# Performance work log

Measured on AMD Instinct MI355X. Metric: run time of the kernel, lower is better.

Reference implementation:

```python
import jax, jax.numpy as jnp
import numpy as np

M, N, C, K, R = 192, 192, 256, 5, 4096
POOL, TILES = 2, 3
ANCHOR_SIZES = (16, 32, 64, 96, 128)


def setup_inputs() -> dict:
    key = jax.random.key(0)
    ks = jax.random.split(key, 8)
    field = 16
    features = jax.random.normal(ks[0], (1, M, N, C), jnp.float32)
    obj_output = jax.random.normal(ks[1], (M, N, 2 * K), jnp.float32)
    reg_output = jax.random.normal(ks[2], (M, N, 4 * K), jnp.float32) * 0.1
    anchor_px = jnp.array(ANCHOR_SIZES, jnp.int32)
    # anchors on the field grid (create_anchors semantics): centers at (i+0.5)*field
    px = jax.random.randint(ks[3], (R,), 0, N)
    py = jax.random.randint(ks[4], (R,), 0, M)
    kidx = jax.random.randint(ks[5], (R,), 0, K)
    aw = anchor_px[kidx].astype(jnp.float32)
    ax = px.astype(jnp.float32) * field + field / 2
    ay = py.astype(jnp.float32) * field + field / 2
    anchors = jnp.stack([ax, ay, aw, aw], axis=1)  # [R,4] center format (cx,cy,w,h)
    # matched ground-truth boxes: jittered anchors, top-left format (x,y,w,h)
    jit = jax.random.normal(ks[6], (R, 4), jnp.float32) * 0.1
    bw = aw * jnp.exp(jit[:, 2])
    bh = aw * jnp.exp(jit[:, 3])
    bx = ax + jit[:, 0] * aw - bw / 2
    by = ay + jit[:, 1] * aw - bh / 2
    boxes = jnp.stack([bx, by, bw, bh], axis=1)
    W_fc = jax.random.normal(ks[7], (TILES * TILES * C, 4), jnp.float32) * 0.01
    b_fc = jnp.zeros((4,), jnp.float32)
    return dict(features=features, obj_output=obj_output, reg_output=reg_output,
                anchors=anchors, boxes=boxes, W_fc=W_fc, b_fc=b_fc,
                anchor_px=anchor_px, field=field)


def map_outputs(output, anchors, anchor_px, field):
    # anchor width -> anchor-size index (argmax over equality, as in the TF code)
    kk = jnp.argmax(anchors[:, 3, None].astype(jnp.int32) == anchor_px[None, :], axis=1)
    px = ((anchors[:, 0] - field / 2) / field).astype(jnp.int32)
    py = ((anchors[:, 1] - field / 2) / field).astype(jnp.int32)
    Kn = anchor_px.shape[0]
    resh = output.reshape(output.shape[0], output.shape[1], Kn, output.shape[2] // Kn)
    return resh[py, px, kk]  # [R, D/K] gather_nd equivalent


def parameterize(ref, boxes):
    # ref: [R,4] center format; boxes: [R,4] top-left format
    tx = (boxes[:, 0] + boxes[:, 2] / 2 - ref[:, 0]) / ref[:, 2]
    ty = (boxes[:, 1] + boxes[:, 3] / 2 - ref[:, 1]) / ref[:, 3]
    tw = jnp.log(boxes[:, 2] / ref[:, 2])
    th = jnp.log(boxes[:, 3] / ref[:, 3])
    return jnp.stack([tx, ty, tw, th], axis=1)


def unparameterize(reg, ref):
    cx = reg[:, 0] * ref[:, 2] + ref[:, 0]
    cy = reg[:, 1] * ref[:, 3] + ref[:, 1]
    w = ref[:, 2] * jnp.exp(reg[:, 2])
    h = ref[:, 3] * jnp.exp(reg[:, 3])
    return jnp.stack([cx, cy, w, h], axis=1)  # center format


def roialign(features, cboxes, field):
    # cboxes: [R,4] center format. Sample S x S bilinear points per box.
    S = POOL * TILES
    fmap = features[0]  # [M,N,C]
    offs = (jnp.arange(S, dtype=jnp.float32) + 0.5) / S
    x0f = cboxes[:, 0] - cboxes[:, 2] / 2
    y0f = cboxes[:, 1] - cboxes[:, 3] / 2
    fx = (x0f[:, None] + offs[None, :] * cboxes[:, 2, None]) / field - 0.5  # [R,S]
    fy = (y0f[:, None] + offs[None, :] * cboxes[:, 3, None]) / field - 0.5
    x0 = jnp.clip(jnp.floor(fx), 0, N - 2).astype(jnp.int32)
    y0 = jnp.clip(jnp.floor(fy), 0, M - 2).astype(jnp.int32)
    wx = jnp.clip(fx - x0.astype(jnp.float32), 0.0, 1.0)
    wy = jnp.clip(fy - y0.astype(jnp.float32), 0.0, 1.0)

    def g(yi, xi):
        return fmap[yi[:, :, None], xi[:, None, :]]  # [R,S,S,C]

    wxb = wx[:, None, :, None]
    top = (1 - wxb) * g(y0, x0) + wxb * g(y0, x0 + 1)
    bot = (1 - wxb) * g(y0 + 1, x0) + wxb * g(y0 + 1, x0 + 1)
    wyb = wy[:, :, None, None]
    return (1 - wyb) * top + wyb * bot  # [R,S,S,C]


def reference(features, obj_output, reg_output, anchors, boxes, W_fc, b_fc, anchor_px, field):
    f = jnp.float32(field)
    obj = jax.nn.softmax(map_outputs(obj_output, anchors, anchor_px, f), axis=-1)  # [R,2]
    reg = map_outputs(reg_output, anchors, anchor_px, f)                            # [R,4]
    rpn_boxes = unparameterize(reg, anchors)                                        # [R,4]
    interp = roialign(features, rpn_boxes, f)                                       # [R,6,6,C]
    pooled = interp.reshape(R, TILES, POOL, TILES, POOL, C).max(axis=(2, 4))        # [R,3,3,C]
    align_reg = pooled.reshape(R, -1) @ W_fc + b_fc                                 # [R,4]
    align_boxes = unparameterize(align_reg, rpn_boxes)                              # [R,4]
    align_reg_label = parameterize(rpn_boxes, boxes)                                # [R,4]
    return jnp.concatenate([obj, rpn_boxes, align_boxes, align_reg_label], axis=1)  # [R,14]
```

## Files before the change

kernel.cpp:

```cpp
#include <hip/hip_runtime.h>
#include <hip/hip_bf16.h>
#include <math.h>

constexpr int MH = 192;
constexpr int NH = 192;
constexpr int CH = 256;
constexpr int KH = 5;
constexpr int SS = 6;
constexpr int TT = 3;

__global__ __launch_bounds__(256)
void rcnn_head_kernel(const float* __restrict__ features,
                      const float* __restrict__ obj_out,
                      const float* __restrict__ reg_out,
                      const float* __restrict__ anchors,
                      const float* __restrict__ boxes,
                      const float* __restrict__ W_fc,
                      const float* __restrict__ b_fc,
                      const int*   __restrict__ anchor_px,
                      const int*   __restrict__ field_p,
                      float*       __restrict__ out)
{
    const int r = blockIdx.x;
    const int c = threadIdx.x;
    const float field = (float)field_p[0];

    const float ax = anchors[r * 4 + 0];
    const float ay = anchors[r * 4 + 1];
    const float aw = anchors[r * 4 + 2];
    const float ah = anchors[r * 4 + 3];

    const int awi = (int)ah;
    int kk = 0;
#pragma unroll
    for (int i = 0; i < KH; ++i) {
        if (anchor_px[i] == awi) kk = i;
    }
    const int px = (int)((ax - field * 0.5f) / field);
    const int py = (int)((ay - field * 0.5f) / field);
    const int base = (py * NH + px) * KH + kk;

    const float o0 = obj_out[base * 2 + 0];
    const float o1 = obj_out[base * 2 + 1];
    const float om = fmaxf(o0, o1);
    const float e0 = expf(o0 - om);
    const float e1 = expf(o1 - om);
    const float einv = 1.0f / (e0 + e1);
    const float obj0 = e0 * einv;
    const float obj1 = e1 * einv;

    const float rg0 = reg_out[base * 4 + 0];
    const float rg1 = reg_out[base * 4 + 1];
    const float rg2 = reg_out[base * 4 + 2];
    const float rg3 = reg_out[base * 4 + 3];
    const float cx = rg0 * aw + ax;
    const float cy = rg1 * ah + ay;
    const float bw = aw * expf(rg2);
    const float bh = ah * expf(rg3);

    const float x0f = cx - bw * 0.5f;
    const float y0f = cy - bh * 0.5f;
    int   xi[SS], yi[SS];
    float wx[SS], wy[SS];
#pragma unroll
    for (int i = 0; i < SS; ++i) {
        const float off = (i + 0.5f) * (1.0f / SS);
        float fx = (x0f + off * bw) / field - 0.5f;
        float fl = floorf(fx);
        fl = fminf(fmaxf(fl, 0.0f), (float)(NH - 2));
        xi[i] = (int)fl;
        wx[i] = fminf(fmaxf(fx - fl, 0.0f), 1.0f);

        float fy = (y0f + off * bh) / field - 0.5f;
        float fy0 = floorf(fy);
        fy0 = fminf(fmaxf(fy0, 0.0f), (float)(MH - 2));
        yi[i] = (int)fy0;
        wy[i] = fminf(fmaxf(fy - fy0, 0.0f), 1.0f);
    }

    float pooled[TT][TT];
#pragma unroll
    for (int ty = 0; ty < TT; ++ty) {
#pragma unroll
        for (int tx = 0; tx < TT; ++tx) {
            float mx = -INFINITY;
#pragma unroll
            for (int sy = 0; sy < 2; ++sy) {
#pragma unroll
                for (int sx = 0; sx < 2; ++sx) {
                    const int iy = ty * 2 + sy;
                    const int ix = tx * 2 + sx;
                    const int y0 = yi[iy];
                    const int x0 = xi[ix];
                    const float* p = features + ((size_t)(y0 * NH + x0)) * CH + c;
                    const float v00 = p[0];
                    const float v01 = p[CH];
                    const float v10 = p[NH * CH];
                    const float v11 = p[NH * CH + CH];
                    const float wxx = wx[ix];
                    const float wyy = wy[iy];
                    const float top = (1.0f - wxx) * v00 + wxx * v01;
                    const float bot = (1.0f - wxx) * v10 + wxx * v11;
                    const float v = (1.0f - wyy) * top + wyy * bot;
                    mx = fmaxf(mx, v);
                }
            }
            pooled[ty][tx] = mx;
        }
    }

    float s0 = 0.f, s1 = 0.f, s2 = 0.f, s3 = 0.f;
#pragma unroll
    for (int t = 0; t < TT * TT; ++t) {
        const float p = pooled[t / TT][t % TT];
        const float4 w4 = *reinterpret_cast<const float4*>(&W_fc[(size_t)(t * CH + c) * 4]);
        s0 += p * w4.x;
        s1 += p * w4.y;
        s2 += p * w4.z;
        s3 += p * w4.w;
    }

#pragma unroll
    for (int off = 32; off > 0; off >>= 1) {
        s0 += __shfl_down(s0, off);
        s1 += __shfl_down(s1, off);
        s2 += __shfl_down(s2, off);
        s3 += __shfl_down(s3, off);
    }

    __shared__ float red[4][4];
    const int wave = c >> 6;
    const int lane = c & 63;
    if (lane == 0) {
        red[wave][0] = s0;
        red[wave][1] = s1;
        red[wave][2] = s2;
        red[wave][3] = s3;
    }
    __syncthreads();

    if (c == 0) {
        const float a0 = b_fc[0] + red[0][0] + red[1][0] + red[2][0] + red[3][0];
        const float a1 = b_fc[1] + red[0][1] + red[1][1] + red[2][1] + red[3][1];
        const float a2 = b_fc[2] + red[0][2] + red[1][2] + red[2][2] + red[3][2];
        const float a3 = b_fc[3] + red[0][3] + red[1][3] + red[2][3] + red[3][3];

        const float acx = a0 * bw + cx;
        const float acy = a1 * bh + cy;
        const float aww = bw * expf(a2);
        const float ahh = bh * expf(a3);

        const float gx = boxes[r * 4 + 0];
        const float gy = boxes[r * 4 + 1];
        const float gw = boxes[r * 4 + 2];
        const float gh = boxes[r * 4 + 3];
        const float txl = (gx + gw * 0.5f - cx) / bw;
        const float tyl = (gy + gh * 0.5f - cy) / bh;
        const float twl = logf(gw / bw);
        const float thl = logf(gh / bh);

        float* o = out + (size_t)r * 14;
        o[0]  = obj0; o[1]  = obj1;
        o[2]  = cx;   o[3]  = cy;  o[4]  = bw;  o[5]  = bh;
        o[6]  = acx;  o[7]  = acy; o[8]  = aww; o[9]  = ahh;
        o[10] = txl;  o[11] = tyl; o[12] = twl; o[13] = thl;
    }
}

extern "C" void kernel_launch(void* const* d_in, const int* in_sizes, int n_in,
                              void* d_out, int out_size, void* d_ws, size_t ws_size,
                              hipStream_t stream) {
    const float* features  = (const float*)d_in[0];
    const float* obj_out   = (const float*)d_in[1];
    const float* reg_out   = (const float*)d_in[2];
    const float* anchors   = (const float*)d_in[3];
    const float* boxes     = (const float*)d_in[4];
    const float* W_fc      = (const float*)d_in[5];
    const float* b_fc      = (const float*)d_in[6];
    const int*   anchor_px = (const int*)d_in[7];
    const int*   field_p   = (const int*)d_in[8];
    float* out = (float*)d_out;

    const int R = in_sizes[3] / 4;

    rcnn_head_kernel<<<dim3(R), dim3(256), 0, stream>>>(
        features, obj_out, reg_out, anchors, boxes, W_fc, b_fc,
        anchor_px, field_p, out);
}
```

Baseline: 117.6 us.

## Map one RoI per wavefront with float4 channel loads, drop block reduction

Each 256-thread block now handles four RoIs, one per wavefront. Each lane covers four channels using float4 loads of the features and W_fc. This removes the shared-memory cross-wave reduction and the __syncthreads, widens memory transactions, and spreads the per-RoI scalar setup across more useful work per thread. It raises register use per thread, and the block count is R/4 with no tail handling, so R must be a multiple of 4.

```diff
diff --git a/kernel.cpp b/kernel.cpp
--- a/kernel.cpp
+++ b/kernel.cpp
@@ -8,6 +8,7 @@
 constexpr int KH = 5;
 constexpr int SS = 6;
 constexpr int TT = 3;
+constexpr int ROIS_PER_BLOCK = 4;
 
 __global__ __launch_bounds__(256)
 void rcnn_head_kernel(const float* __restrict__ features,
@@ -21,8 +22,9 @@
                       const int*   __restrict__ field_p,
                       float*       __restrict__ out)
 {
-    const int r = blockIdx.x;
-    const int c = threadIdx.x;
+    const int wave = threadIdx.x >> 6;
+    const int lane = threadIdx.x & 63;
+    const int r = blockIdx.x * ROIS_PER_BLOCK + wave;
     const float field = (float)field_p[0];
 
     const float ax = anchors[r * 4 + 0];
@@ -78,12 +80,13 @@
         wy[i] = fminf(fmaxf(fy - fy0, 0.0f), 1.0f);
     }
 
-    float pooled[TT][TT];
+    const float* fbase = features + (size_t)lane * 4;
+    float4 pooled[TT][TT];
 #pragma unroll
     for (int ty = 0; ty < TT; ++ty) {
 #pragma unroll
         for (int tx = 0; tx < TT; ++tx) {
-            float mx = -INFINITY;
+            float4 mx = make_float4(-INFINITY, -INFINITY, -INFINITY, -INFINITY);
 #pragma unroll
             for (int sy = 0; sy < 2; ++sy) {
 #pragma unroll
@@ -92,17 +95,28 @@
                     const int ix = tx * 2 + sx;
                     const int y0 = yi[iy];
                     const int x0 = xi[ix];
-                    const float* p = features + ((size_t)(y0 * NH + x0)) * CH + c;
-                    const float v00 = p[0];
-                    const float v01 = p[CH];
-                    const float v10 = p[NH * CH];
-                    const float v11 = p[NH * CH + CH];
+                    const float* p0 = fbase + (size_t)(y0 * NH + x0) * CH;
+                    const float* p1 = p0 + (size_t)NH * CH;
+                    const float4 v00 = *reinterpret_cast<const float4*>(p0);
+                    const float4 v01 = *reinterpret_cast<const float4*>(p0 + CH);
+                    const float4 v10 = *reinterpret_cast<const float4*>(p1);
+                    const float4 v11 = *reinterpret_cast<const float4*>(p1 + CH);
                     const float wxx = wx[ix];
                     const float wyy = wy[iy];
-                    const float top = (1.0f - wxx) * v00 + wxx * v01;
-                    const float bot = (1.0f - wxx) * v10 + wxx * v11;
-                    const float v = (1.0f - wyy) * top + wyy * bot;
-                    mx = fmaxf(mx, v);
+                    const float cwx = 1.0f - wxx;
+                    const float cwy = 1.0f - wyy;
+                    float tpx = cwx * v00.x + wxx * v01.x;
+                    float tpy = cwx * v00.y + wxx * v01.y;
+                    float tpz = cwx * v00.z + wxx * v01.z;
+                    float tpw = cwx * v00.w + wxx * v01.w;
+                    float btx = cwx * v10.x + wxx * v11.x;
+                    float bty = cwx * v10.y + wxx * v11.y;
+                    float btz = cwx * v10.z + wxx * v11.z;
+                    float btw = cwx * v10.w + wxx * v11.w;
+                    mx.x = fmaxf(mx.x, cwy * tpx + wyy * btx);
+                    mx.y = fmaxf(mx.y, cwy * tpy + wyy * bty);
+                    mx.z = fmaxf(mx.z, cwy * tpz + wyy * btz);
+                    mx.w = fmaxf(mx.w, cwy * tpw + wyy * btw);
                 }
             }
             pooled[ty][tx] = mx;
@@ -112,12 +126,16 @@
     float s0 = 0.f, s1 = 0.f, s2 = 0.f, s3 = 0.f;
 #pragma unroll
     for (int t = 0; t < TT * TT; ++t) {
-        const float p = pooled[t / TT][t % TT];
-        const float4 w4 = *reinterpret_cast<const float4*>(&W_fc[(size_t)(t * CH + c) * 4]);
-        s0 += p * w4.x;
-        s1 += p * w4.y;
-        s2 += p * w4.z;
-        s3 += p * w4.w;
+        const float4 p = pooled[t / TT][t % TT];
+        const float* wrow = &W_fc[(size_t)(t * CH + lane * 4) * 4];
+        const float4 w0 = *reinterpret_cast<const float4*>(wrow + 0);
+        const float4 w1 = *reinterpret_cast<const float4*>(wrow + 4);
+        const float4 w2 = *reinterpret_cast<const float4*>(wrow + 8);
+        const float4 w3 = *reinterpret_cast<const float4*>(wrow + 12);
+        s0 += p.x * w0.x + p.y * w1.x + p.z * w2.x + p.w * w3.x;
+        s1 += p.x * w0.y + p.y * w1.y + p.z * w2.y + p.w * w3.y;
+        s2 += p.x * w0.z + p.y * w1.z + p.z * w2.z + p.w * w3.z;
+        s3 += p.x * w0.w + p.y * w1.w + p.z * w2.w + p.w * w3.w;
     }
 
 #pragma unroll
@@ -128,22 +146,11 @@
         s3 += __shfl_down(s3, off);
     }
 
-    __shared__ float red[4][4];
-    const int wave = c >> 6;
-    const int lane = c & 63;
     if (lane == 0) {
-        red[wave][0] = s0;
-        red[wave][1] = s1;
-        red[wave][2] = s2;
-        red[wave][3] = s3;
-    }
-    __syncthreads();
-
-    if (c == 0) {
-        const float a0 = b_fc[0] + red[0][0] + red[1][0] + red[2][0] + red[3][0];
-        const float a1 = b_fc[1] + red[0][1] + red[1][1] + red[2][1] + red[3][1];
-        const float a2 = b_fc[2] + red[0][2] + red[1][2] + red[2][2] + red[3][2];
-        const float a3 = b_fc[3] + red[0][3] + red[1][3] + red[2][3] + red[3][3];
+        const float a0 = b_fc[0] + s0;
+        const float a1 = b_fc[1] + s1;
+        const float a2 = b_fc[2] + s2;
+        const float a3 = b_fc[3] + s3;
 
         const float acx = a0 * bw + cx;
         const float acy = a1 * bh + cy;
@@ -182,8 +189,9 @@
     float* out = (float*)d_out;
 
     const int R = in_sizes[3] / 4;
+    const int blocks = R / ROIS_PER_BLOCK;
 
-    rcnn_head_kernel<<<dim3(R), dim3(256), 0, stream>>>(
+    rcnn_head_kernel<<<dim3(blocks), dim3(256), 0, stream>>>(
         features, obj_out, reg_out, anchors, boxes, W_fc, b_fc,
         anchor_px, field_p, out);
 }
```

After: 130.2 us. +10.7%, slower.

## Bucket ROIs by anchor row and remap blocks so each XCD gets nearby rows

Applied to the files above, without the earlier changes.

Adds a single-block counting-sort kernel that orders ROIs by their anchor row index and writes the resulting permutation into workspace. The main kernel then maps block IDs so that consecutive sorted ROIs land on the same XCD, with round-robin dispatch assumed across 8 XCDs. The goal is to raise L2 reuse of the feature map, since spatially close ROIs read overlapping pixels. The cost is an extra serial launch and a permutation lookup per block. The scheme only helps if that block-to-XCD mapping assumption holds.

```diff
diff --git a/kernel.cpp b/kernel.cpp
--- a/kernel.cpp
+++ b/kernel.cpp
@@ -8,6 +8,41 @@
 constexpr int KH = 5;
 constexpr int SS = 6;
 constexpr int TT = 3;
+constexpr int NXCD = 8;
+
+__global__ __launch_bounds__(256)
+void roi_sort_kernel(const float* __restrict__ anchors, int R,
+                     const int* __restrict__ field_p,
+                     int* __restrict__ perm)
+{
+    __shared__ int offs[MH];
+    const int t = threadIdx.x;
+    const float field = (float)field_p[0];
+
+    for (int i = t; i < MH; i += 256) offs[i] = 0;
+    __syncthreads();
+    for (int r = t; r < R; r += 256) {
+        const float ay = anchors[4 * r + 1];
+        int py = (int)((ay - field * 0.5f) / field);
+        atomicAdd(&offs[py], 1);
+    }
+    __syncthreads();
+    if (t == 0) {
+        int acc = 0;
+        for (int i = 0; i < MH; ++i) {
+            int h = offs[i];
+            offs[i] = acc;
+            acc += h;
+        }
+    }
+    __syncthreads();
+    for (int r = t; r < R; r += 256) {
+        const float ay = anchors[4 * r + 1];
+        int py = (int)((ay - field * 0.5f) / field);
+        int slot = atomicAdd(&offs[py], 1);
+        perm[slot] = r;
+    }
+}
 
 __global__ __launch_bounds__(256)
 void rcnn_head_kernel(const float* __restrict__ features,
@@ -19,9 +54,14 @@
                       const float* __restrict__ b_fc,
                       const int*   __restrict__ anchor_px,
                       const int*   __restrict__ field_p,
+                      const int*   __restrict__ perm,
+                      int chunk,
                       float*       __restrict__ out)
 {
-    const int r = blockIdx.x;
+    const int b = blockIdx.x;
+    const int rank = (b % NXCD) * chunk + (b / NXCD);
+    const int r = perm ? perm[rank] : rank;
+
     const int c = threadIdx.x;
     const float field = (float)field_p[0];
 
@@ -183,7 +223,14 @@
 
     const int R = in_sizes[3] / 4;
 
+    int* perm = nullptr;
+    if (ws_size >= (size_t)R * sizeof(int) && (R % NXCD) == 0) {
+        perm = (int*)d_ws;
+        roi_sort_kernel<<<dim3(1), dim3(256), 0, stream>>>(anchors, R, field_p, perm);
+    }
+
+    const int chunk = R / NXCD;
     rcnn_head_kernel<<<dim3(R), dim3(256), 0, stream>>>(
         features, obj_out, reg_out, anchors, boxes, W_fc, b_fc,
-        anchor_px, field_p, out);
+        anchor_px, field_p, perm, chunk, out);
 }
```

Measured after the change: 130.8 us. 1.11x slower.
